# Optimization experiments

Measured on AMD Instinct MI355X. Metric: run time of the kernel, lower is better.

The kernel has to match this reference:

```python
import jax, jax.numpy as jnp
import numpy as np

GAMMA = 0.9


def setup_inputs() -> dict:
    key = jax.random.key(0)
    k1, k2 = jax.random.split(key)
    B, H, W, C, D = 1, 32, 32, 8, 64
    num_heads = 8
    head_dim = D // num_heads  # 8, must equal C for the module's broadcasting
    x = jax.random.normal(k1, (B, H, W, C, D), dtype=jnp.float32)
    decay = jnp.ones((1, num_heads, 1, 1, 1), dtype=jnp.float32)  # base_decay=1.0
    spec_pe = jax.random.normal(k2, (1, num_heads, 1, 1, head_dim), dtype=jnp.float32)
    return {"x": x, "decay": decay, "spec_pe": spec_pe}


def _manhattan_mask(H, W, C, dtype):
    # dist[h1,w1,c1,h2,w2,c2] = |h1-h2| + |w1-w2| + |c1-c2|
    # Built from per-axis |delta| tables to avoid the (H,W,C,H,W,C,3) intermediate.
    dh = jnp.abs(jnp.arange(H)[:, None] - jnp.arange(H)[None, :])  # (H,H)
    dw = jnp.abs(jnp.arange(W)[:, None] - jnp.arange(W)[None, :])  # (W,W)
    dc = jnp.abs(jnp.arange(C)[:, None] - jnp.arange(C)[None, :])  # (C,C)
    dist = (dh[:, None, None, :, None, None]
            + dw[None, :, None, None, :, None]
            + dc[None, None, :, None, None, :])  # (H,W,C,H,W,C)
    mask = jnp.asarray(GAMMA, dtype) ** dist.astype(dtype)
    return mask[None, None]  # (1,1,H,W,C,H,W,C)


def reference(x, decay, spec_pe):
    B, H, W, C, D = x.shape
    mask = _manhattan_mask(H, W, C, x.dtype)            # (1,1,H,W,C,H,W,C)
    mean = jnp.mean(mask, axis=(5, 6, 7), keepdims=True)  # (1,1,H,W,C,1,1,1)
    # spec_pe (1,nh,1,1,Dh) broadcasts against trailing dims (requires nh==C, Dh==C)
    spec = spec_pe * mean
    mask = mask * (1.0 + spec)
    mask = mask * decay  # decay (1,nh,1,1,1) broadcasts at dim -4 (nh==C)
    return mask
```

## Files before the change

kernel.cpp:

```cpp
#include <hip/hip_runtime.h>


constexpr int TOTAL_F4 = 16777216;

__global__ __launch_bounds__(256) void manhattan_relpos_kernel(
    const float* __restrict__ decay,
    const float* __restrict__ spec_pe,
    float* __restrict__ out)
{
    __shared__ float powtab[72];
    __shared__ float Sh[32];
    __shared__ float meanC[8];
    __shared__ float A[64];
    __shared__ float SP[64];

    const int tid = threadIdx.x;

    if (tid < 72) {
        powtab[tid] = exp2f((float)tid * -0.15200309344504997f);
    }
    __syncthreads();
    if (tid < 32) {
        float s = 0.0f;
        #pragma unroll
        for (int j = 0; j < 32; ++j) s += powtab[abs(tid - j)];
        Sh[tid] = s;
    } else if (tid < 40) {
        const int c1 = tid - 32;
        float s = 0.0f;
        #pragma unroll
        for (int j = 0; j < 8; ++j) s += powtab[abs(c1 - j)];
        meanC[c1] = s * (1.0f / 8192.0f);
    } else if (tid >= 64 && tid < 128) {
        const int i = tid - 64;
        const int c1 = i >> 3, c2 = i & 7;
        A[i]  = powtab[abs(c1 - c2)] * decay[c1];
        SP[i] = spec_pe[i];
    }
    __syncthreads();

    const int stride = gridDim.x * blockDim.x;
    for (int idx = blockIdx.x * blockDim.x + tid; idx < TOTAL_F4; idx += stride) {
        const int half = idx & 1;
        const int w2 = (idx >> 1)  & 31;
        const int h2 = (idx >> 6)  & 31;
        const int c1 = (idx >> 11) & 7;
        const int w1 = (idx >> 14) & 31;
        const int h1 = (idx >> 19) & 31;

        const float p = powtab[abs(h1 - h2) + abs(w1 - w2)];
        const float m = Sh[h1] * Sh[w1] * meanC[c1];
        const int cbase = (c1 << 3) + (half << 2);

        float4 v;
        v.x = p * A[cbase + 0] * fmaf(SP[cbase + 0], m, 1.0f);
        v.y = p * A[cbase + 1] * fmaf(SP[cbase + 1], m, 1.0f);
        v.z = p * A[cbase + 2] * fmaf(SP[cbase + 2], m, 1.0f);
        v.w = p * A[cbase + 3] * fmaf(SP[cbase + 3], m, 1.0f);
        reinterpret_cast<float4*>(out)[idx] = v;
    }
}

extern "C" void kernel_launch(void* const* d_in, const int* in_sizes, int n_in,
                              void* d_out, int out_size, void* d_ws, size_t ws_size,
                              hipStream_t stream) {
    const float* decay   = (const float*)d_in[1];
    const float* spec_pe = (const float*)d_in[2];
    float* out = (float*)d_out;

    dim3 grid(8192), block(256);
    manhattan_relpos_kernel<<<grid, block, 0, stream>>>(decay, spec_pe, out);
}
```

Baseline: 256.9 us.

## Assign one (h1,w1) per block, precompute per-c factors, use nontemporal stores

Each block now owns a single (h1,w1) pair. It precomputes a 32x32 spatial decay table and a 64-entry channel factor E that folds decay, spec_pe and the mean term, so each output vector is a single multiply. Every thread writes 64 float4 outputs with nontemporal stores in place of a grid-stride loop with per-element index decode. This cuts ALU and LDS work in the 256MB write-bound kernel and avoids cache pollution, but the grid shrinks to 1024 blocks and each block carries more setup.

```diff
diff --git a/kernel.cpp b/kernel.cpp
--- a/kernel.cpp
+++ b/kernel.cpp
@@ -1,7 +1,7 @@
 #include <hip/hip_runtime.h>
 
 
-constexpr int TOTAL_F4 = 16777216;
+typedef float f32x4 __attribute__((ext_vector_type(4)));
 
 __global__ __launch_bounds__(256) void manhattan_relpos_kernel(
     const float* __restrict__ decay,
@@ -9,55 +9,64 @@
     float* __restrict__ out)
 {
     __shared__ float powtab[72];
-    __shared__ float Sh[32];
-    __shared__ float meanC[8];
-    __shared__ float A[64];
-    __shared__ float SP[64];
+    __shared__ float P2d[1024];
+    __shared__ float E[64];
+    __shared__ float mC[8];
+    __shared__ float Ssum[2];
 
     const int tid = threadIdx.x;
+    const int h1 = blockIdx.x >> 5;
+    const int w1 = blockIdx.x & 31;
 
-    if (tid < 72) {
+    if (tid < 72)
         powtab[tid] = exp2f((float)tid * -0.15200309344504997f);
+    __syncthreads();
+
+    #pragma unroll
+    for (int k = 0; k < 4; ++k) {
+        const int i  = tid + (k << 8);
+        const int h2 = i >> 5, w2 = i & 31;
+        P2d[i] = powtab[abs(h1 - h2) + abs(w1 - w2)];
     }
-    __syncthreads();
-    if (tid < 32) {
+    if (tid < 2) {
+        const int a = tid ? w1 : h1;
         float s = 0.0f;
         #pragma unroll
-        for (int j = 0; j < 32; ++j) s += powtab[abs(tid - j)];
-        Sh[tid] = s;
-    } else if (tid < 40) {
-        const int c1 = tid - 32;
+        for (int j = 0; j < 32; ++j) s += powtab[abs(a - j)];
+        Ssum[tid] = s;
+    } else if (tid >= 8 && tid < 16) {
+        const int c1 = tid - 8;
         float s = 0.0f;
         #pragma unroll
         for (int j = 0; j < 8; ++j) s += powtab[abs(c1 - j)];
-        meanC[c1] = s * (1.0f / 8192.0f);
-    } else if (tid >= 64 && tid < 128) {
-        const int i = tid - 64;
-        const int c1 = i >> 3, c2 = i & 7;
-        A[i]  = powtab[abs(c1 - c2)] * decay[c1];
-        SP[i] = spec_pe[i];
+        mC[c1] = s * (1.0f / 8192.0f);
     }
     __syncthreads();
 
-    const int stride = gridDim.x * blockDim.x;
-    for (int idx = blockIdx.x * blockDim.x + tid; idx < TOTAL_F4; idx += stride) {
-        const int half = idx & 1;
-        const int w2 = (idx >> 1)  & 31;
-        const int h2 = (idx >> 6)  & 31;
-        const int c1 = (idx >> 11) & 7;
-        const int w1 = (idx >> 14) & 31;
-        const int h1 = (idx >> 19) & 31;
+    if (tid < 64) {
+        const int c1 = tid >> 3, c2 = tid & 7;
+        const float m = Ssum[0] * Ssum[1] * mC[c1];
+        E[tid] = powtab[abs(c1 - c2)] * decay[c1] * fmaf(spec_pe[tid], m, 1.0f);
+    }
+    __syncthreads();
 
-        const float p = powtab[abs(h1 - h2) + abs(w1 - w2)];
-        const float m = Sh[h1] * Sh[w1] * meanC[c1];
-        const int cbase = (c1 << 3) + (half << 2);
+    const int half  = tid & 1;
+    const int pbase = ((tid >> 6) << 5) + ((tid >> 1) & 31);
+    f32x4* out4 = reinterpret_cast<f32x4*>(out) + ((size_t)blockIdx.x << 14) + tid;
+    const f32x4* E4 = reinterpret_cast<const f32x4*>(E);
 
-        float4 v;
-        v.x = p * A[cbase + 0] * fmaf(SP[cbase + 0], m, 1.0f);
-        v.y = p * A[cbase + 1] * fmaf(SP[cbase + 1], m, 1.0f);
-        v.z = p * A[cbase + 2] * fmaf(SP[cbase + 2], m, 1.0f);
-        v.w = p * A[cbase + 3] * fmaf(SP[cbase + 3], m, 1.0f);
-        reinterpret_cast<float4*>(out)[idx] = v;
+    float pr[8];
+    #pragma unroll
+    for (int hh = 0; hh < 8; ++hh) pr[hh] = P2d[pbase + (hh << 7)];
+
+    #pragma unroll
+    for (int c1 = 0; c1 < 8; ++c1) {
+        const f32x4 e = E4[(c1 << 1) + half];
+        #pragma unroll
+        for (int hh = 0; hh < 8; ++hh) {
+            const f32x4 v = pr[hh] * e;
+            __builtin_nontemporal_store(v, out4 + (c1 << 11) + (hh << 8));
+        }
     }
 }
 
@@ -68,6 +77,6 @@
     const float* spec_pe = (const float*)d_in[2];
     float* out = (float*)d_out;
 
-    dim3 grid(8192), block(256);
+    dim3 grid(1024), block(256);
     manhattan_relpos_kernel<<<grid, block, 0, stream>>>(decay, spec_pe, out);
 }
```

Result: slower. 266.0 us (+3.5%).
